# Kernel tuning notes

Hardware: AMD Instinct MI355X
Metric: run time of the kernel (lower is better)

The kernel has to match this reference:

```python
import jax, jax.numpy as jnp
import numpy as np

B, SQ, SK, H, A = 4, 512, 512, 256, 128

def setup_inputs() -> dict:
    key = jax.random.key(0)
    ks = jax.random.split(key, 8)
    s = 1.0 / np.sqrt(H)
    sa = 1.0 / np.sqrt(A)
    return {
        "Q": jax.random.normal(ks[0], (B, SQ, H), dtype=jnp.float32),
        "K": jax.random.normal(ks[1], (B, SK, H), dtype=jnp.float32),
        "V": jax.random.normal(ks[2], (B, SK, H), dtype=jnp.float32),
        "W_q": jax.random.uniform(ks[3], (H, A), jnp.float32, -s, s),
        "W_k": jax.random.uniform(ks[4], (H, A), jnp.float32, -s, s),
        "v": jax.random.uniform(ks[5], (A,), jnp.float32, -sa, sa),
        "W_o": jax.random.uniform(ks[6], (H, H), jnp.float32, -s, s),
        "b_o": jax.random.uniform(ks[7], (H,), jnp.float32, -s, s),
    }

def reference(Q, K, V, W_q, W_k, v, W_o, b_o):
    # Q: (B, Sq, H), K/V: (B, Sk, H)
    Qt = Q @ W_q                      # (B, Sq, A)
    Kt = K @ W_k                      # (B, Sk, A)
    additive = jnp.tanh(Qt[:, :, None, :] + Kt[:, None, :, :])  # (B, Sq, Sk, A)
    scores = jnp.einsum('bqka,a->bqk', additive, v)             # (B, Sq, Sk)
    weights = jax.nn.softmax(scores, axis=-1)                   # (B, Sq, Sk)
    out = jnp.einsum('bqk,bkh->bqh', weights, V)                 # (B, Sq, H)
    out = out @ W_o + b_o
    return (out, weights)
```

## Files before the change

kernel.cpp:

```cpp
#include <hip/hip_runtime.h>
#include <math.h>

#define BB 4
#define SQL 512
#define SKL 512
#define HH 256
#define AA 128

#define PRESCALE 2.8853900817779268f
#define LOG2E    1.4426950408889634f

__device__ inline void fma4(float4& a, float s, const float4& b) {
    a.x = fmaf(s, b.x, a.x); a.y = fmaf(s, b.y, a.y);
    a.z = fmaf(s, b.z, a.z); a.w = fmaf(s, b.w, a.w);
}

template <int CTRL>
__device__ __forceinline__ float dpp_add(float x) {
    int m = __builtin_amdgcn_update_dpp(__float_as_int(x), __float_as_int(x),
                                        CTRL, 0xF, 0xF, false);
    return x + __int_as_float(m);
}
__device__ __forceinline__ float red16(float x) {
    x = dpp_add<0xB1>(x);
    x = dpp_add<0x4E>(x);
    x = dpp_add<0x141>(x);
    x = dpp_add<0x140>(x);
    return x;
}

#define PIN4(V) asm volatile("" : "+v"((V).x), "+v"((V).y), "+v"((V).z), "+v"((V).w))

__global__ __launch_bounds__(256) void prep_kernel(
    const float* __restrict__ Q, const float* __restrict__ K,
    const float* __restrict__ V,
    const float* __restrict__ Wq, const float* __restrict__ Wk,
    const float* __restrict__ Wo,
    float* __restrict__ Qt, float* __restrict__ Kt, float* __restrict__ VW)
{
    __shared__ float rows[16 * HH];
    __shared__ float wl[64 * 128];
    int tid = threadIdx.x;
    int bid = blockIdx.x;

    const float* X; const float* W; float* Y;
    int ldW, ldY, col0, r0; float scale;
    if (bid < 128)      { X=Q; W=Wq; Y=Qt; ldW=AA; ldY=AA; col0=0; r0=bid*16;       scale=PRESCALE; }
    else if (bid < 256) { X=K; W=Wk; Y=Kt; ldW=AA; ldY=AA; col0=0; r0=(bid-128)*16; scale=PRESCALE; }
    else { int b2=bid-256; X=V; W=Wo; Y=VW; ldW=HH; ldY=HH; col0=(b2&1)*128; r0=(b2>>1)*16; scale=1.0f; }

    {
        const float4* Xv = (const float4*)(X + (size_t)r0 * HH);
        float4* rv = (float4*)rows;
        rv[tid]       = Xv[tid];
        rv[tid + 256] = Xv[tid + 256];
        rv[tid + 512] = Xv[tid + 512];
        rv[tid + 768] = Xv[tid + 768];
    }

    int r  = tid >> 5;
    int c4 = tid & 31;
    float4 accA = {0.f,0.f,0.f,0.f}, accB = {0.f,0.f,0.f,0.f};

    for (int ch = 0; ch < 4; ++ch) {
        __syncthreads();
        {
            const float* Wbase = W + (size_t)(ch * 64) * ldW + col0;
            float4* wv = (float4*)wl;
            #pragma unroll
            for (int it = 0; it < 8; ++it) {
                int l = tid + it * 256;
                wv[l] = *(const float4*)(Wbase + (size_t)(l >> 5) * ldW + ((l & 31) << 2));
            }
        }
        __syncthreads();
        const float* rrowA = rows + r * HH + ch * 64;
        const float* rrowB = rows + (r + 8) * HH + ch * 64;
        #pragma unroll 4
        for (int h4 = 0; h4 < 16; ++h4) {
            float4 ra = *(const float4*)(rrowA + h4 * 4);
            float4 rb = *(const float4*)(rrowB + h4 * 4);
            const float* wbase = wl + (h4 * 4) * 128 + (c4 << 2);
            float4 w0 = *(const float4*)(wbase);
            float4 w1 = *(const float4*)(wbase + 128);
            float4 w2 = *(const float4*)(wbase + 256);
            float4 w3 = *(const float4*)(wbase + 384);
            fma4(accA, ra.x, w0); fma4(accA, ra.y, w1);
            fma4(accA, ra.z, w2); fma4(accA, ra.w, w3);
            fma4(accB, rb.x, w0); fma4(accB, rb.y, w1);
            fma4(accB, rb.z, w2); fma4(accB, rb.w, w3);
        }
    }
    accA.x *= scale; accA.y *= scale; accA.z *= scale; accA.w *= scale;
    accB.x *= scale; accB.y *= scale; accB.z *= scale; accB.w *= scale;
    if (bid < 256) {
        accA.x = __builtin_amdgcn_exp2f(accA.x); accA.y = __builtin_amdgcn_exp2f(accA.y);
        accA.z = __builtin_amdgcn_exp2f(accA.z); accA.w = __builtin_amdgcn_exp2f(accA.w);
        accB.x = __builtin_amdgcn_exp2f(accB.x); accB.y = __builtin_amdgcn_exp2f(accB.y);
        accB.z = __builtin_amdgcn_exp2f(accB.z); accB.w = __builtin_amdgcn_exp2f(accB.w);
    }
    *(float4*)(Y + (size_t)(r0 + r)     * ldY + col0 + (c4 << 2)) = accA;
    *(float4*)(Y + (size_t)(r0 + r + 8) * ldY + col0 + (c4 << 2)) = accB;
}

#define FORQ(OP) OP(0) OP(1) OP(2) OP(3) OP(4) OP(5) OP(6) OP(7)

__global__ __launch_bounds__(512)
__attribute__((amdgpu_waves_per_eu(2, 2)))
void score_kernel(
    const float* __restrict__ Qt, const float* __restrict__ Kt,
    const float* __restrict__ v,  const float* __restrict__ VW,
    const float* __restrict__ bo,
    float* __restrict__ weights,  float* __restrict__ out)
{
    __shared__ float score[8][SKL];
    __shared__ float pout[8][4][HH];

    int tid = threadIdx.x;
    int b  = blockIdx.x >> 6;
    int q0 = (blockIdx.x & 63) << 3;
    int ag = tid & 15;
    int kl = tid >> 4;

    float4 v2a, v2b;
    {
        const float4* vp = (const float4*)(v + ag * 8);
        v2a = vp[0]; v2b = vp[1];
        v2a.x *= 2.f; v2a.y *= 2.f; v2a.z *= 2.f; v2a.w *= 2.f;
        v2b.x *= 2.f; v2b.y *= 2.f; v2b.z *= 2.f; v2b.w *= 2.f;
        PIN4(v2a); PIN4(v2b);
    }

#define DECL_EQ(Qi) float4 EqA##Qi, EqB##Qi;
    FORQ(DECL_EQ)
#define LOAD_EQ(Qi) { \
        const float4* qp = (const float4*)(Qt + (size_t)(b * SQL + q0 + Qi) * AA + ag * 8); \
        (EqA##Qi) = qp[0]; (EqB##Qi) = qp[1]; \
        PIN4(EqA##Qi); PIN4(EqB##Qi); }
    FORQ(LOAD_EQ)

    float S_all;
    {
        float ls = (v2a.x + v2a.y) + (v2a.z + v2a.w)
                 + (v2b.x + v2b.y) + (v2b.z + v2b.w);
        S_all = 0.5f * red16(ls);
    }

    const float4* ktp = (const float4*)(Kt + (size_t)b * SKL * AA);

    {
        float4 ka = ktp[(size_t)kl * (AA / 4) + ag * 2];
        float4 kb = ktp[(size_t)kl * (AA / 4) + ag * 2 + 1];
        #pragma unroll 1
        for (int c = 0; c < 16; ++c) {
            float4 na, nb;
            if (c < 15) {
                int kn = (c + 1) * 32 + kl;
                na = ktp[(size_t)kn * (AA / 4) + ag * 2];
                nb = ktp[(size_t)kn * (AA / 4) + ag * 2 + 1];
            }
#define DECL_P(Qi) float p##Qi = 0.f;
            FORQ(DECL_P)
#define STEPC(KE, VE, HB, COMP) { \
            float Ek = KE; \
            p0 = fmaf(VE, __builtin_amdgcn_rcpf(fmaf(Ek, (Eq##HB##0).COMP, 1.0f)), p0); \
            p1 = fmaf(VE, __builtin_amdgcn_rcpf(fmaf(Ek, (Eq##HB##1).COMP, 1.0f)), p1); \
            p2 = fmaf(VE, __builtin_amdgcn_rcpf(fmaf(Ek, (Eq##HB##2).COMP, 1.0f)), p2); \
            p3 = fmaf(VE, __builtin_amdgcn_rcpf(fmaf(Ek, (Eq##HB##3).COMP, 1.0f)), p3); \
            p4 = fmaf(VE, __builtin_amdgcn_rcpf(fmaf(Ek, (Eq##HB##4).COMP, 1.0f)), p4); \
            p5 = fmaf(VE, __builtin_amdgcn_rcpf(fmaf(Ek, (Eq##HB##5).COMP, 1.0f)), p5); \
            p6 = fmaf(VE, __builtin_amdgcn_rcpf(fmaf(Ek, (Eq##HB##6).COMP, 1.0f)), p6); \
            p7 = fmaf(VE, __builtin_amdgcn_rcpf(fmaf(Ek, (Eq##HB##7).COMP, 1.0f)), p7); }
            STEPC(ka.x, v2a.x, A, x) STEPC(ka.y, v2a.y, A, y)
            STEPC(ka.z, v2a.z, A, z) STEPC(ka.w, v2a.w, A, w)
            STEPC(kb.x, v2b.x, B, x) STEPC(kb.y, v2b.y, B, y)
            STEPC(kb.z, v2b.z, B, z) STEPC(kb.w, v2b.w, B, w)
#define RED_P(Qi) p##Qi = red16(p##Qi);
            FORQ(RED_P)
            if (ag == 0) {
                int k = c * 32 + kl;
#define STORE_P(Qi) score[Qi][k] = (S_all - p##Qi) * LOG2E;
                FORQ(STORE_P)
            }
            ka = na; kb = nb;
        }
    }
    __syncthreads();

    int wave = tid >> 6, lane = tid & 63;
    {
        int qi = wave;
        float ssum = 0.f;
        #pragma unroll
        for (int it = 0; it < 2; ++it) {
            int k0 = it * 256 + (lane << 2);
            float4 sv = *(float4*)&score[qi][k0];
            sv.x = __builtin_amdgcn_exp2f(sv.x);
            sv.y = __builtin_amdgcn_exp2f(sv.y);
            sv.z = __builtin_amdgcn_exp2f(sv.z);
            sv.w = __builtin_amdgcn_exp2f(sv.w);
            *(float4*)&score[qi][k0] = sv;
            ssum += (sv.x + sv.y) + (sv.z + sv.w);
        }
        #pragma unroll
        for (int off = 32; off; off >>= 1) ssum += __shfl_xor(ssum, off);
        float rinv = 1.0f / ssum;
        size_t rowoff = (size_t)(b * SQL + q0 + qi) * SKL;
        #pragma unroll
        for (int it = 0; it < 2; ++it) {
            int k0 = it * 256 + (lane << 2);
            float4 sv = *(float4*)&score[qi][k0];
            sv.x *= rinv; sv.y *= rinv; sv.z *= rinv; sv.w *= rinv;
            *(float4*)&score[qi][k0] = sv;
            *(float4*)(weights + rowoff + k0) = sv;
        }
    }
    __syncthreads();

#define DECL_ACC(Qi) float4 acc##Qi = {0.f, 0.f, 0.f, 0.f};
    FORQ(DECL_ACC)
    {
        const float4* VWb = (const float4*)(VW + (size_t)b * SKL * HH);
        int kbase = wave * 64;
        #pragma unroll 2
        for (int k4 = 0; k4 < 16; ++k4) {
            int kk = kbase + k4 * 4;
#define DECL_W(Qi) float4 w##Qi = *(const float4*)&score[Qi][kk];
            FORQ(DECL_W)
            float4 vw;
            vw = VWb[(size_t)(kk + 0) * (HH / 4) + lane];
#define FMA_X(Qi) fma4(acc##Qi, (w##Qi).x, vw);
            FORQ(FMA_X)
            vw = VWb[(size_t)(kk + 1) * (HH / 4) + lane];
#define FMA_Y(Qi) fma4(acc##Qi, (w##Qi).y, vw);
            FORQ(FMA_Y)
            vw = VWb[(size_t)(kk + 2) * (HH / 4) + lane];
#define FMA_Z(Qi) fma4(acc##Qi, (w##Qi).z, vw);
            FORQ(FMA_Z)
            vw = VWb[(size_t)(kk + 3) * (HH / 4) + lane];
#define FMA_W(Qi) fma4(acc##Qi, (w##Qi).w, vw);
            FORQ(FMA_W)
        }
    }

    int h  = tid & 255;
    int qh = tid >> 8;
    float bias = bo[h];

    *(float4*)&pout[wave][0][lane << 2] = acc0;
    *(float4*)&pout[wave][1][lane << 2] = acc1;
    *(float4*)&pout[wave][2][lane << 2] = acc2;
    *(float4*)&pout[wave][3][lane << 2] = acc3;
    __syncthreads();
    #pragma unroll
    for (int qq = 0; qq < 2; ++qq) {
        int qi = qh * 2 + qq;
        float s = bias;
        #pragma unroll
        for (int w2 = 0; w2 < 8; ++w2) s += pout[w2][qi][h];
        out[(size_t)(b * SQL + q0 + qi) * HH + h] = s;
    }
    __syncthreads();

    *(float4*)&pout[wave][0][lane << 2] = acc4;
    *(float4*)&pout[wave][1][lane << 2] = acc5;
    *(float4*)&pout[wave][2][lane << 2] = acc6;
    *(float4*)&pout[wave][3][lane << 2] = acc7;
    __syncthreads();
    #pragma unroll
    for (int qq = 0; qq < 2; ++qq) {
        int qi = qh * 2 + qq;
        float s = bias;
        #pragma unroll
        for (int w2 = 0; w2 < 8; ++w2) s += pout[w2][qi][h];
        out[(size_t)(b * SQL + q0 + 4 + qi) * HH + h] = s;
    }
}

extern "C" void kernel_launch(void* const* d_in, const int* in_sizes, int n_in,
                              void* d_out, int out_size, void* d_ws, size_t ws_size,
                              hipStream_t stream)
{
    const float* Q  = (const float*)d_in[0];
    const float* K  = (const float*)d_in[1];
    const float* V  = (const float*)d_in[2];
    const float* Wq = (const float*)d_in[3];
    const float* Wk = (const float*)d_in[4];
    const float* v  = (const float*)d_in[5];
    const float* Wo = (const float*)d_in[6];
    const float* bo = (const float*)d_in[7];

    float* out     = (float*)d_out;
    float* weights = out + (size_t)BB * SQL * HH;

    float* Qt = (float*)d_ws;
    float* Kt = Qt + (size_t)BB * SQL * AA;
    float* VW = Kt + (size_t)BB * SKL * AA;

    prep_kernel <<<512, 256, 0, stream>>>(Q, K, V, Wq, Wk, Wo, Qt, Kt, VW);
    score_kernel<<<256, 512, 0, stream>>>(Qt, Kt, v, VW, bo, weights, out);
}
```

Before: 119.2 us.

## Halve queries per block to 4 and double grid to 512 blocks

```diff
diff --git a/kernel.cpp b/kernel.cpp
--- a/kernel.cpp
+++ b/kernel.cpp
@@ -103,22 +103,21 @@
     *(float4*)(Y + (size_t)(r0 + r + 8) * ldY + col0 + (c4 << 2)) = accB;
 }
 
-#define FORQ(OP) OP(0) OP(1) OP(2) OP(3) OP(4) OP(5) OP(6) OP(7)
-
-__global__ __launch_bounds__(512)
-__attribute__((amdgpu_waves_per_eu(2, 2)))
-void score_kernel(
+#define FORQ4(OP) OP(0) OP(1) OP(2) OP(3)
+
+__global__ __launch_bounds__(512) void score_kernel(
     const float* __restrict__ Qt, const float* __restrict__ Kt,
     const float* __restrict__ v,  const float* __restrict__ VW,
     const float* __restrict__ bo,
     float* __restrict__ weights,  float* __restrict__ out)
 {
-    __shared__ float score[8][SKL];
+    __shared__ float score[4][SKL];
     __shared__ float pout[8][4][HH];
+    __shared__ float ssums[2][4];
 
     int tid = threadIdx.x;
-    int b  = blockIdx.x >> 6;
-    int q0 = (blockIdx.x & 63) << 3;
+    int b  = blockIdx.x >> 7;
+    int q0 = (blockIdx.x & 127) << 2;
     int ag = tid & 15;
     int kl = tid >> 4;
 
@@ -132,12 +131,12 @@
     }
 
 #define DECL_EQ(Qi) float4 EqA##Qi, EqB##Qi;
-    FORQ(DECL_EQ)
+    FORQ4(DECL_EQ)
 #define LOAD_EQ(Qi) { \
         const float4* qp = (const float4*)(Qt + (size_t)(b * SQL + q0 + Qi) * AA + ag * 8); \
         (EqA##Qi) = qp[0]; (EqB##Qi) = qp[1]; \
         PIN4(EqA##Qi); PIN4(EqB##Qi); }
-    FORQ(LOAD_EQ)
+    FORQ4(LOAD_EQ)
 
     float S_all;
     {
@@ -159,28 +158,24 @@
                 na = ktp[(size_t)kn * (AA / 4) + ag * 2];
                 nb = ktp[(size_t)kn * (AA / 4) + ag * 2 + 1];
             }
-#define DECL_P(Qi) float p##Qi = 0.f;
-            FORQ(DECL_P)
+            float p0 = 0.f, p1 = 0.f, p2 = 0.f, p3 = 0.f;
 #define STEPC(KE, VE, HB, COMP) { \
             float Ek = KE; \
             p0 = fmaf(VE, __builtin_amdgcn_rcpf(fmaf(Ek, (Eq##HB##0).COMP, 1.0f)), p0); \
             p1 = fmaf(VE, __builtin_amdgcn_rcpf(fmaf(Ek, (Eq##HB##1).COMP, 1.0f)), p1); \
             p2 = fmaf(VE, __builtin_amdgcn_rcpf(fmaf(Ek, (Eq##HB##2).COMP, 1.0f)), p2); \
-            p3 = fmaf(VE, __builtin_amdgcn_rcpf(fmaf(Ek, (Eq##HB##3).COMP, 1.0f)), p3); \
-            p4 = fmaf(VE, __builtin_amdgcn_rcpf(fmaf(Ek, (Eq##HB##4).COMP, 1.0f)), p4); \
-            p5 = fmaf(VE, __builtin_amdgcn_rcpf(fmaf(Ek, (Eq##HB##5).COMP, 1.0f)), p5); \
-            p6 = fmaf(VE, __builtin_amdgcn_rcpf(fmaf(Ek, (Eq##HB##6).COMP, 1.0f)), p6); \
-            p7 = fmaf(VE, __builtin_amdgcn_rcpf(fmaf(Ek, (Eq##HB##7).COMP, 1.0f)), p7); }
+            p3 = fmaf(VE, __builtin_amdgcn_rcpf(fmaf(Ek, (Eq##HB##3).COMP, 1.0f)), p3); }
             STEPC(ka.x, v2a.x, A, x) STEPC(ka.y, v2a.y, A, y)
             STEPC(ka.z, v2a.z, A, z) STEPC(ka.w, v2a.w, A, w)
             STEPC(kb.x, v2b.x, B, x) STEPC(kb.y, v2b.y, B, y)
             STEPC(kb.z, v2b.z, B, z) STEPC(kb.w, v2b.w, B, w)
-#define RED_P(Qi) p##Qi = red16(p##Qi);
-            FORQ(RED_P)
+            p0 = red16(p0); p1 = red16(p1); p2 = red16(p2); p3 = red16(p3);
             if (ag == 0) {
                 int k = c * 32 + kl;
-#define STORE_P(Qi) score[Qi][k] = (S_all - p##Qi) * LOG2E;
-                FORQ(STORE_P)
+                score[0][k] = (S_all - p0) * LOG2E;
+                score[1][k] = (S_all - p1) * LOG2E;
+                score[2][k] = (S_all - p2) * LOG2E;
+                score[3][k] = (S_all - p3) * LOG2E;
             }
             ka = na; kb = nb;
         }
@@ -188,92 +183,73 @@
     __syncthreads();
 
     int wave = tid >> 6, lane = tid & 63;
-    {
-        int qi = wave;
-        float ssum = 0.f;
-        #pragma unroll
-        for (int it = 0; it < 2; ++it) {
-            int k0 = it * 256 + (lane << 2);
-            float4 sv = *(float4*)&score[qi][k0];
-            sv.x = __builtin_amdgcn_exp2f(sv.x);
-            sv.y = __builtin_amdgcn_exp2f(sv.y);
-            sv.z = __builtin_amdgcn_exp2f(sv.z);
-            sv.w = __builtin_amdgcn_exp2f(sv.w);
-            *(float4*)&score[qi][k0] = sv;
-            ssum += (sv.x + sv.y) + (sv.z + sv.w);
-        }
+    int qi = wave & 3;
+    int kh = wave >> 2;
+    {
+        int k0 = kh * 256 + (lane << 2);
+        float4 sv = *(float4*)&score[qi][k0];
+        sv.x = __builtin_amdgcn_exp2f(sv.x);
+        sv.y = __builtin_amdgcn_exp2f(sv.y);
+        sv.z = __builtin_amdgcn_exp2f(sv.z);
+        sv.w = __builtin_amdgcn_exp2f(sv.w);
+        *(float4*)&score[qi][k0] = sv;
+        float ssum = (sv.x + sv.y) + (sv.z + sv.w);
         #pragma unroll
         for (int off = 32; off; off >>= 1) ssum += __shfl_xor(ssum, off);
-        float rinv = 1.0f / ssum;
+        if (lane == 0) ssums[kh][qi] = ssum;
+    }
+    __syncthreads();
+    {
+        float rinv = 1.0f / (ssums[0][qi] + ssums[1][qi]);
+        int k0 = kh * 256 + (lane << 2);
+        float4 sv = *(float4*)&score[qi][k0];
+        sv.x *= rinv; sv.y *= rinv; sv.z *= rinv; sv.w *= rinv;
+        *(float4*)&score[qi][k0] = sv;
         size_t rowoff = (size_t)(b * SQL + q0 + qi) * SKL;
-        #pragma unroll
-        for (int it = 0; it < 2; ++it) {
-            int k0 = it * 256 + (lane << 2);
-            float4 sv = *(float4*)&score[qi][k0];
-            sv.x *= rinv; sv.y *= rinv; sv.z *= rinv; sv.w *= rinv;
-            *(float4*)&score[qi][k0] = sv;
-            *(float4*)(weights + rowoff + k0) = sv;
-        }
-    }
-    __syncthreads();
-
-#define DECL_ACC(Qi) float4 acc##Qi = {0.f, 0.f, 0.f, 0.f};
-    FORQ(DECL_ACC)
+        *(float4*)(weights + rowoff + k0) = sv;
+    }
+    __syncthreads();
+
+    float4 acc0 = {0,0,0,0}, acc1 = {0,0,0,0}, acc2 = {0,0,0,0}, acc3 = {0,0,0,0};
     {
         const float4* VWb = (const float4*)(VW + (size_t)b * SKL * HH);
         int kbase = wave * 64;
         #pragma unroll 2
         for (int k4 = 0; k4 < 16; ++k4) {
             int kk = kbase + k4 * 4;
-#define DECL_W(Qi) float4 w##Qi = *(const float4*)&score[Qi][kk];
-            FORQ(DECL_W)
+            float4 w0 = *(const float4*)&score[0][kk];
+            float4 w1 = *(const float4*)&score[1][kk];
+            float4 w2 = *(const float4*)&score[2][kk];
+            float4 w3 = *(const float4*)&score[3][kk];
             float4 vw;
             vw = VWb[(size_t)(kk + 0) * (HH / 4) + lane];
-#define FMA_X(Qi) fma4(acc##Qi, (w##Qi).x, vw);
-            FORQ(FMA_X)
+            fma4(acc0, w0.x, vw); fma4(acc1, w1.x, vw); fma4(acc2, w2.x, vw); fma4(acc3, w3.x, vw);
             vw = VWb[(size_t)(kk + 1) * (HH / 4) + lane];
-#define FMA_Y(Qi) fma4(acc##Qi, (w##Qi).y, vw);
-            FORQ(FMA_Y)
+            fma4(acc0, w0.y, vw); fma4(acc1, w1.y, vw); fma4(acc2, w2.y, vw); fma4(acc3, w3.y, vw);
             vw = VWb[(size_t)(kk + 2) * (HH / 4) + lane];
-#define FMA_Z(Qi) fma4(acc##Qi, (w##Qi).z, vw);
-            FORQ(FMA_Z)
+            fma4(acc0, w0.z, vw); fma4(acc1, w1.z, vw); fma4(acc2, w2.z, vw); fma4(acc3, w3.z, vw);
             vw = VWb[(size_t)(kk + 3) * (HH / 4) + lane];
-#define FMA_W(Qi) fma4(acc##Qi, (w##Qi).w, vw);
-            FORQ(FMA_W)
-        }
-    }
-
-    int h  = tid & 255;
-    int qh = tid >> 8;
-    float bias = bo[h];
+            fma4(acc0, w0.w, vw); fma4(acc1, w1.w, vw); fma4(acc2, w2.w, vw); fma4(acc3, w3.w, vw);
+        }
+    }
 
     *(float4*)&pout[wave][0][lane << 2] = acc0;
     *(float4*)&pout[wave][1][lane << 2] = acc1;
     *(float4*)&pout[wave][2][lane << 2] = acc2;
     *(float4*)&pout[wave][3][lane << 2] = acc3;
     __syncthreads();
-    #pragma unroll
-    for (int qq = 0; qq < 2; ++qq) {
-        int qi = qh * 2 + qq;
-        float s = bias;
+    {
+        int h  = tid & 255;
+        int qh = tid >> 8;
+        float bias = bo[h];
         #pragma unroll
-        for (int w2 = 0; w2 < 8; ++w2) s += pout[w2][qi][h];
-        out[(size_t)(b * SQL + q0 + qi) * HH + h] = s;
-    }
-    __syncthreads();
-
-    *(float4*)&pout[wave][0][lane << 2] = acc4;
-    *(float4*)&pout[wave][1][lane << 2] = acc5;
-    *(float4*)&pout[wave][2][lane << 2] = acc6;
-    *(float4*)&pout[wave][3][lane << 2] = acc7;
-    __syncthreads();
-    #pragma unroll
-    for (int qq = 0; qq < 2; ++qq) {
-        int qi = qh * 2 + qq;
-        float s = bias;
-        #pragma unroll
-        for (int w2 = 0; w2 < 8; ++w2) s += pout[w2][qi][h];
-        out[(size_t)(b * SQL + q0 + 4 + qi) * HH + h] = s;
+        for (int qq = 0; qq < 2; ++qq) {
+            int qi2 = qh * 2 + qq;
+            float s = bias;
+            #pragma unroll
+            for (int w2 = 0; w2 < 8; ++w2) s += pout[w2][qi2][h];
+            out[(size_t)(b * SQL + q0 + qi2) * HH + h] = s;
+        }
     }
 }
 
@@ -298,5 +274,5 @@
     float* VW = Kt + (size_t)BB * SKL * AA;
 
     prep_kernel <<<512, 256, 0, stream>>>(Q, K, V, Wq, Wk, Wo, Qt, Kt, VW);
-    score_kernel<<<256, 512, 0, stream>>>(Qt, Kt, v, VW, bo, weights, out);
-}
+    score_kernel<<<512, 512, 0, stream>>>(Qt, Kt, v, VW, bo, weights, out);
+}
```

New measurement: 118.7 us. About the same (-0.3%).
